# Kernel optimization log

Hardware: AMD Instinct MI355X
Metric: run time of the kernel (lower is better)

The kernel has to match this reference:

```python
import jax, jax.numpy as jnp
import numpy as np

B, T, C, H = 4, 2048, 1024, 16
HS = C // H  # head dim = 64
EPS = 1e-5


def _layernorm(h, w, b):
    m = jnp.mean(h, axis=-1, keepdims=True)
    v = jnp.mean(jnp.square(h - m), axis=-1, keepdims=True)
    return (h - m) * jax.lax.rsqrt(v + EPS) * w + b


def _quantize_int8(t):
    # per-tensor absmax int8 quantization, matching the torch code
    absmax = jnp.max(jnp.abs(t))
    scale = jnp.where(absmax > 0, absmax / 127.0, jnp.float32(1.0))
    q = jnp.clip(jnp.round(t / scale), -127, 127).astype(jnp.int8)
    return q, scale


def setup_inputs() -> dict:
    key = jax.random.key(0)
    ks = jax.random.split(key, 8)
    w = lambda k, shape: (jax.random.normal(k, shape, jnp.float32) * 0.02)
    return {
        "x": jax.random.normal(ks[0], (B, T, C), jnp.float32),
        "ln1_w": jnp.ones((C,), jnp.float32),
        "ln1_b": jnp.zeros((C,), jnp.float32),
        "W_qkv": w(ks[1], (C, 3 * C)),
        "b_qkv": jnp.zeros((3 * C,), jnp.float32),
        "W_o": w(ks[2], (C, C)),
        "b_o": jnp.zeros((C,), jnp.float32),
        "ln2_w": jnp.ones((C,), jnp.float32),
        "ln2_b": jnp.zeros((C,), jnp.float32),
        "W_fc": w(ks[3], (C, 4 * C)),
        "b_fc": jnp.zeros((4 * C,), jnp.float32),
        "W_pr": w(ks[4], (4 * C, C)),
        "b_pr": jnp.zeros((C,), jnp.float32),
    }


def reference(x, ln1_w, ln1_b, W_qkv, b_qkv, W_o, b_o, ln2_w, ln2_b, W_fc, b_fc, W_pr, b_pr):
    # ---- attention (prefill, cache-owner, kv_cache_quant=True, use_cache=True) ----
    h = _layernorm(x, ln1_w, ln1_b)
    qkv = h @ W_qkv + b_qkv                       # (B,T,3C)
    q, k, v = jnp.split(qkv, 3, axis=-1)
    q = q.reshape(B, T, H, HS).transpose(0, 2, 1, 3)  # (B,H,T,hs)
    k = k.reshape(B, T, H, HS).transpose(0, 2, 1, 3)
    v = v.reshape(B, T, H, HS).transpose(0, 2, 1, 3)

    # quantized `present` cache (returned, not used for attention in prefill path)
    k_quant, k_scale = _quantize_int8(k)
    v_quant, v_scale = _quantize_int8(v)

    # causal SDPA (dropout=0)
    att = jnp.einsum("bhqd,bhkd->bhqk", q, k) * (1.0 / np.sqrt(HS))
    causal = jnp.tril(jnp.ones((T, T), bool))
    att = jnp.where(causal[None, None], att, jnp.float32(-jnp.inf))
    att = jax.nn.softmax(att, axis=-1)
    y = jnp.einsum("bhqk,bhkd->bhqd", att, v)
    y = y.transpose(0, 2, 1, 3).reshape(B, T, C)
    y = y @ W_o + b_o
    x = x + y

    # ---- MLP ----
    h2 = _layernorm(x, ln2_w, ln2_b)
    h2 = jax.nn.gelu(h2 @ W_fc + b_fc, approximate=False)
    x = x + (h2 @ W_pr + b_pr)

    return x, k_quant, k_scale, v_quant, v_scale
```

## Files before the change

### kernel.cpp

```cpp
#include <hip/hip_runtime.h>
#include <cmath>

typedef __bf16 bf16;
typedef float f32x4 __attribute__((ext_vector_type(4)));
typedef __bf16 bf16x4 __attribute__((ext_vector_type(4)));
typedef __bf16 bf16x8 __attribute__((ext_vector_type(8)));

#define DEVI __device__ __forceinline__

constexpr int Bn = 4, Tn = 2048, Cn = 1024, Hn = 16, HSn = 64;
constexpr int C3n = 3 * Cn;
constexpr int BTn = Bn * Tn;

constexpr size_t OFF_WT_QKV = 0;
constexpr size_t OFF_WT_O   = 6291456;
constexpr size_t OFF_WT_FC  = 8388608;
constexpr size_t OFF_WT_PR  = 16777216;
constexpr size_t OFF_H      = 25165824;
constexpr size_t OFF_Y      = 41943040;
constexpr size_t OFF_X1     = 58720256;
constexpr size_t OFF_AMAX   = 92274688;
constexpr size_t OFF_QKV    = 92274944;
constexpr size_t OFF_G      = OFF_QKV;

constexpr size_t OUT_X  = 0;
constexpr size_t OUT_KQ = 8388608;
constexpr size_t OUT_KS = 16777216;
constexpr size_t OUT_VQ = 16777217;
constexpr size_t OUT_VS = 25165825;

DEVI void g2l16(const void* g, void* l) {
  __builtin_amdgcn_global_load_lds(
      (__attribute__((address_space(1))) void*)g,
      (__attribute__((address_space(3))) void*)l, 16, 0, 0);
}

DEVI float gelu_f(float x) {
  const float ax = fabsf(x) * 0.7071067811865476f;
  const float t = 1.0f / (1.0f + 0.3275911f * ax);
  const float p = t * (0.254829592f + t * (-0.284496736f +
                  t * (1.421413741f + t * (-1.453152027f + t * 1.061405429f))));
  float er = 1.0f - p * __expf(-ax * ax);
  er = (x < 0.0f) ? -er : er;
  return 0.5f * x * (1.0f + er);
}

struct TrJob { const float* W; bf16* Wt; int K, N, bx; };

__global__ __launch_bounds__(256) void k_prep(const float* W0, bf16* T0,
                                              const float* W1, bf16* T1,
                                              const float* W2, bf16* T2,
                                              const float* W3, bf16* T3,
                                              unsigned int* amax) {
  __shared__ float tile[32][33];
  const int id = blockIdx.x;
  if (id == 0 && threadIdx.x == 0 && threadIdx.y == 0) { amax[0] = 0u; amax[1] = 0u; }

  const float* W; bf16* Wt; int K, N, lid;
  if (id < 3072)      { W = W0; Wt = T0; K = 1024; N = 3072; lid = id; }
  else if (id < 4096) { W = W1; Wt = T1; K = 1024; N = 1024; lid = id - 3072; }
  else if (id < 8192) { W = W2; Wt = T2; K = 1024; N = 4096; lid = id - 4096; }
  else                { W = W3; Wt = T3; K = 4096; N = 1024; lid = id - 8192; }
  const int gx = N >> 5;
  const int n0 = (lid % gx) * 32, k0 = (lid / gx) * 32;
  const int tx = threadIdx.x, ty = threadIdx.y;
#pragma unroll
  for (int i = 0; i < 4; ++i) {
    int k = k0 + ty + i * 8;
    tile[ty + i * 8][tx] = W[(size_t)k * N + (n0 + tx)];
  }
  __syncthreads();
#pragma unroll
  for (int i = 0; i < 4; ++i) {
    int n = n0 + ty + i * 8;
    Wt[(size_t)n * K + (k0 + tx)] = (bf16)tile[tx][ty + i * 8];
  }
}

__global__ __launch_bounds__(256) void k_ln(const float* __restrict__ x,
                                            const float* __restrict__ g,
                                            const float* __restrict__ b,
                                            bf16* __restrict__ out) {
  __shared__ float red[8];
  const int row = blockIdx.x, tid = threadIdx.x;
  const int lane = tid & 63, wv = tid >> 6;
  f32x4 v = ((const f32x4*)(x + (size_t)row * Cn))[tid];

  float s = v[0] + v[1] + v[2] + v[3];
  s += __shfl_down(s, 32); s += __shfl_down(s, 16); s += __shfl_down(s, 8);
  s += __shfl_down(s, 4);  s += __shfl_down(s, 2);  s += __shfl_down(s, 1);
  if (!lane) red[wv] = s;
  __syncthreads();
  const float mean = (red[0] + red[1] + red[2] + red[3]) * (1.0f / 1024.0f);
  __syncthreads();

  f32x4 d = v - mean;
  float s2 = d[0]*d[0] + d[1]*d[1] + d[2]*d[2] + d[3]*d[3];
  s2 += __shfl_down(s2, 32); s2 += __shfl_down(s2, 16); s2 += __shfl_down(s2, 8);
  s2 += __shfl_down(s2, 4);  s2 += __shfl_down(s2, 2);  s2 += __shfl_down(s2, 1);
  if (!lane) red[wv] = s2;
  __syncthreads();
  const float var = (red[0] + red[1] + red[2] + red[3]) * (1.0f / 1024.0f);
  const float inv = rsqrtf(var + 1e-5f);

  f32x4 gw = ((const f32x4*)g)[tid];
  f32x4 bb = ((const f32x4*)b)[tid];
  bf16x4 o;
#pragma unroll
  for (int j = 0; j < 4; ++j) o[j] = (bf16)(d[j] * inv * gw[j] + bb[j]);
  *(bf16x4*)(out + (size_t)row * Cn + tid * 4) = o;
}

#define VMCNT(N) asm volatile("s_waitcnt vmcnt(" #N ")" ::: "memory")
#define LGKM0()  asm volatile("s_waitcnt lgkmcnt(0)" ::: "memory")
#define BARW()   asm volatile("s_barrier" ::: "memory")

DEVI void stage_half(const bf16* __restrict__ G, int ldk, int row0, int k0,
                     bf16* dst, int w, int lane) {
  const int srow = lane >> 3;
  const int sch = ((lane & 7) ^ srow) * 8;
  const bf16* src = G + (size_t)(row0 + srow) * ldk + k0 + sch;
#pragma unroll
  for (int i = 0; i < 2; ++i) {
    const int g = 2 * w + i;
    g2l16(src + (size_t)(8 * g) * ldk, dst + g * 512);
  }
}

DEVI void read_b(const bf16* BsB, int wn, int l15, int quad, bf16x8 (&bv)[2][2]) {
#pragma unroll
  for (int nt = 0; nt < 2; ++nt)
#pragma unroll
    for (int kk = 0; kk < 2; ++kk) {
      const int row = wn * 32 + nt * 16 + l15;
      const int c = ((kk * 4 + quad) ^ (l15 & 7)) * 8;
      bv[nt][kk] = *(const bf16x8*)(BsB + row * 64 + c);
    }
}

template <int Q>
DEVI void read_aq(const bf16* AsB, int wm, int l15, int quad, bf16x8 (&af)[2]) {
#pragma unroll
  for (int kk = 0; kk < 2; ++kk) {
    const int row = wm * 64 + Q * 16 + l15;
    const int c = ((kk * 4 + quad) ^ (l15 & 7)) * 8;
    af[kk] = *(const bf16x8*)(AsB + row * 64 + c);
  }
}

template <int Q>
DEVI void mfma_q(const bf16x8 (&af)[2], const bf16x8 (&bv)[2][2],
                 f32x4 (&acc)[4][2]) {
#pragma unroll
  for (int nt = 0; nt < 2; ++nt)
#pragma unroll
    for (int kk = 0; kk < 2; ++kk)
      acc[Q][nt] = __builtin_amdgcn_mfma_f32_16x16x32_bf16(
          af[kk], bv[nt][kk], acc[Q][nt], 0, 0, 0);
}

template <int BUF>
DEVI void tile_iter(int kt, int kIters, const bf16* __restrict__ A,
                    const bf16* __restrict__ Bt, int K, int m0, int n0,
                    bf16* As0, bf16* As1, bf16* Bs0, bf16* Bs1,
                    f32x4 (&acc)[4][2], int w, int lane) {
  const int l15 = lane & 15, quad = lane >> 4;
  const int wm = w >> 2, wn = w & 3;
  const bf16* AsB = BUF ? As1 : As0;
  const bf16* BsB = BUF ? Bs1 : Bs0;
  bf16* AsW = BUF ? As1 : As0;
  bf16* BsW = BUF ? Bs1 : Bs0;

  bf16x8 bv[2][2];
  bf16x8 af0[2], af1[2], af2[2], af3[2];

  read_b(BsB, wn, l15, quad, bv);
  read_aq<0>(AsB, wm, l15, quad, af0);
  read_aq<1>(AsB, wm, l15, quad, af1);
  read_aq<2>(AsB, wm, l15, quad, af2);
  read_aq<3>(AsB, wm, l15, quad, af3);
  mfma_q<0>(af0, bv, acc);
  mfma_q<1>(af1, bv, acc);

  LGKM0();
  BARW();

  if (kt + 2 < kIters) {
    stage_half(A,  K, m0, (kt + 2) * 64, AsW, w, lane);
    stage_half(Bt, K, n0, (kt + 2) * 64, BsW, w, lane);
  }
  mfma_q<2>(af2, bv, acc);
  mfma_q<3>(af3, bv, acc);
  if (kt + 2 < kIters) {
    VMCNT(4);
    BARW();
  } else if (kt + 1 < kIters) {
    VMCNT(0);
    BARW();
  }
}

template <bool RES, bool GELU, bool AMAX, bool F32OUT>
__global__ __launch_bounds__(512, 4) void k_gemmT(const bf16* __restrict__ A,
                                                  const bf16* __restrict__ Bt,
                                                  const float* __restrict__ bias,
                                                  const float* __restrict__ res,
                                                  void* __restrict__ Cout,
                                                  unsigned int* __restrict__ amax,
                                                  int M, int N, int K) {
  __shared__ bf16 As0[128 * 64], As1[128 * 64];
  __shared__ bf16 Bs0[128 * 64], Bs1[128 * 64];
  __shared__ float redA[8];
  const int tid = threadIdx.x;
  const int lane = tid & 63, w = tid >> 6;
  const int wm = w >> 2, wn = w & 3;
  const int l15 = lane & 15, quad = lane >> 4;
  const int m0 = blockIdx.x * 128, n0 = blockIdx.y * 128;
  const int kIters = K >> 6;
  (void)M;

  stage_half(A,  K, m0, 0,  As0, w, lane);
  stage_half(Bt, K, n0, 0,  Bs0, w, lane);
  stage_half(A,  K, m0, 64, As1, w, lane);
  stage_half(Bt, K, n0, 64, Bs1, w, lane);
  VMCNT(4);
  BARW();

  f32x4 acc[4][2] = {};

  const int nPairs = kIters >> 1;
  for (int p = 0; p < nPairs; ++p) {
    tile_iter<0>(2 * p,     kIters, A, Bt, K, m0, n0, As0, As1, Bs0, Bs1, acc, w, lane);
    tile_iter<1>(2 * p + 1, kIters, A, Bt, K, m0, n0, As0, As1, Bs0, Bs1, acc, w, lane);
  }

  const int colB = n0 + wn * 32 + l15;
  const int rowB = m0 + wm * 64 + (quad << 2);
  float lm = 0.0f;
#pragma unroll
  for (int mt = 0; mt < 4; ++mt) {
#pragma unroll
    for (int nt = 0; nt < 2; ++nt) {
      const int col = colB + nt * 16;
      const float bval = bias[col];
#pragma unroll
      for (int r = 0; r < 4; ++r) {
        const int row = rowB + mt * 16 + r;
        float val = acc[mt][nt][r] + bval;
        if (GELU) val = gelu_f(val);
        if (RES)  val += res[(size_t)row * N + col];
        if (AMAX) lm = fmaxf(lm, fabsf(val));
        if (F32OUT) ((float*)Cout)[(size_t)row * N + col] = val;
        else        ((bf16*)Cout)[(size_t)row * N + col] = (bf16)val;
      }
    }
  }

  if (AMAX) {
    const int cls = n0 >> 10;
    if (cls > 0) {
      lm = fmaxf(lm, __shfl_xor(lm, 1));
      lm = fmaxf(lm, __shfl_xor(lm, 2));
      lm = fmaxf(lm, __shfl_xor(lm, 4));
      lm = fmaxf(lm, __shfl_xor(lm, 8));
      lm = fmaxf(lm, __shfl_xor(lm, 16));
      lm = fmaxf(lm, __shfl_xor(lm, 32));
      if (!lane) redA[w] = lm;
      __syncthreads();
      if (tid == 0) {
        float m8 = redA[0];
#pragma unroll
        for (int i = 1; i < 8; ++i) m8 = fmaxf(m8, redA[i]);
        atomicMax(amax + (cls - 1), __float_as_uint(m8));
      }
    }
  }
}

__global__ __launch_bounds__(256) void k_quant(const bf16* __restrict__ qkv,
                                               const unsigned int* __restrict__ amax,
                                               float* __restrict__ out) {
  const float ka = __uint_as_float(amax[0]);
  const float va = __uint_as_float(amax[1]);
  const float ks = ka > 0.0f ? ka / 127.0f : 1.0f;
  const float vs = va > 0.0f ? va / 127.0f : 1.0f;
  if (blockIdx.x == 0 && threadIdx.x == 0) { out[OUT_KS] = ks; out[OUT_VS] = vs; }
  const float kinv = 1.0f / ks, vinv = 1.0f / vs;
  const size_t nchunks = 1048576;
  const size_t stride = (size_t)gridDim.x * blockDim.x;
  for (size_t ci = (size_t)blockIdx.x * blockDim.x + threadIdx.x; ci < nchunks; ci += stride) {
    const int d0 = (int)(ci & 7) * 8;
    const int t  = (int)(ci >> 3) & 2047;
    const int h  = (int)(ci >> 14) & 15;
    const int b  = (int)(ci >> 18);
    const size_t src = ((size_t)(b * Tn + t)) * C3n + h * HSn + d0;
    bf16x8 k8 = *(const bf16x8*)(qkv + src + Cn);
    bf16x8 v8 = *(const bf16x8*)(qkv + src + 2 * Cn);
    float kq[8], vq[8];
#pragma unroll
    for (int j = 0; j < 8; ++j) {
      kq[j] = fminf(fmaxf(rintf((float)k8[j] * kinv), -127.0f), 127.0f);
      vq[j] = fminf(fmaxf(rintf((float)v8[j] * vinv), -127.0f), 127.0f);
    }
    const size_t oi = ci * 8;
    f32x4 a0 = {kq[0], kq[1], kq[2], kq[3]};
    f32x4 a1 = {kq[4], kq[5], kq[6], kq[7]};
    *(f32x4*)(out + OUT_KQ + oi)     = a0;
    *(f32x4*)(out + OUT_KQ + oi + 4) = a1;
    float* vdst = out + OUT_VQ + oi;
#pragma unroll
    for (int j = 0; j < 8; ++j) vdst[j] = vq[j];
  }
}

__global__ __launch_bounds__(256, 3) void k_attn(const bf16* __restrict__ qkv,
                                                 bf16* __restrict__ y) {
  __shared__ bf16 Ks[2][64 * 64];
  __shared__ bf16 Vt[2][64 * 64];
  __shared__ bf16 Pt[4][2][16 * 64];

  const int tid = threadIdx.x;
  const int lane = tid & 63;
  const int w = tid >> 6;
  const int quad = lane >> 4;
  const int l15 = lane & 15;

  const int bh = blockIdx.x;
  const int qt = 15 - (int)blockIdx.y;
  const int b = bh >> 4, h = bh & 15;
  const int q0 = qt * 128;
  const int ktMax = 2 * qt + 1;

  const bf16* qkv_b = qkv + (size_t)b * Tn * C3n + h * HSn;
  const bf16* kbase = qkv_b + Cn;
  const bf16* vbase = qkv_b + 2 * Cn;

  const int srow = lane >> 3;
  const int schunk = ((lane & 7) ^ srow) * 8;

  const bf16* q0p = qkv_b + (size_t)(q0 + 16 * w + l15) * C3n;
  const bf16* q1p = q0p + (size_t)64 * C3n;
  bf16x8 qf[2][2];
  qf[0][0] = *(const bf16x8*)(q0p + quad * 8);
  qf[0][1] = *(const bf16x8*)(q0p + 32 + quad * 8);
  qf[1][0] = *(const bf16x8*)(q1p + quad * 8);
  qf[1][1] = *(const bf16x8*)(q1p + 32 + quad * 8);

  g2l16(kbase + (size_t)(8 * w + srow) * C3n + schunk, (bf16*)Ks[0] + w * 512);
  g2l16(kbase + (size_t)(8 * (w + 4) + srow) * C3n + schunk, (bf16*)Ks[0] + (w + 4) * 512);
  bf16x8 v0 = *(const bf16x8*)(vbase + (size_t)lane * C3n + w * 8);
  bf16x8 v1 = *(const bf16x8*)(vbase + (size_t)lane * C3n + (w + 4) * 8);
  __builtin_amdgcn_s_waitcnt(0);
#pragma unroll
  for (int j = 0; j < 8; ++j) {
    Vt[0][(w * 8 + j) * 64 + ((srow ^ j) << 3) + (lane & 7)] = v0[j];
    Vt[0][((w + 4) * 8 + j) * 64 + ((srow ^ j) << 3) + (lane & 7)] = v1[j];
  }
  __syncthreads();

  f32x4 Od[2][4] = {};
  float m_i[2] = {-INFINITY, -INFINITY};
  float l_i[2] = {0.0f, 0.0f};

  for (int kt = 0; kt <= ktMax; ++kt) {
    const int bsel = kt & 1;

    bf16x8 nv0, nv1;
    if (kt < ktMax) {
      const int kv1 = (kt + 1) * 64;
      g2l16(kbase + (size_t)(kv1 + 8 * w + srow) * C3n + schunk,
            (bf16*)Ks[bsel ^ 1] + w * 512);
      g2l16(kbase + (size_t)(kv1 + 8 * (w + 4) + srow) * C3n + schunk,
            (bf16*)Ks[bsel ^ 1] + (w + 4) * 512);
      nv0 = *(const bf16x8*)(vbase + (size_t)(kv1 + lane) * C3n + w * 8);
      nv1 = *(const bf16x8*)(vbase + (size_t)(kv1 + lane) * C3n + (w + 4) * 8);
    }

    const bf16* KsB = Ks[bsel];
    f32x4 S0[4] = {}, S1[4] = {};
#pragma unroll
    for (int ks = 0; ks < 2; ++ks)
#pragma unroll
      for (int nt = 0; nt < 4; ++nt) {
        const int rn = nt * 16 + l15;
        const int c = ((ks * 4 + quad) ^ (l15 & 7)) * 8;
        bf16x8 kf = *(const bf16x8*)(KsB + rn * 64 + c);
        S0[nt] = __builtin_amdgcn_mfma_f32_16x16x32_bf16(kf, qf[0][ks], S0[nt], 0, 0, 0);
        S1[nt] = __builtin_amdgcn_mfma_f32_16x16x32_bf16(kf, qf[1][ks], S1[nt], 0, 0, 0);
      }

    const int qloc = 16 * w + l15;
    const int th[2] = { kt < 2 * qt ? 64 : (kt == 2 * qt ? qloc : -1),
                        kt < ktMax ? 64 : qloc };
    f32x4* Sg[2] = {S0, S1};
#pragma unroll
    for (int g = 0; g < 2; ++g) {
      float s[4][4];
      float mx = -INFINITY;
#pragma unroll
      for (int nt = 0; nt < 4; ++nt)
#pragma unroll
        for (int r = 0; r < 4; ++r) {
          float v = Sg[g][nt][r] * 0.125f;
          if (nt * 16 + quad * 4 + r > th[g]) v = -INFINITY;
          s[nt][r] = v;
          mx = fmaxf(mx, v);
        }
      mx = fmaxf(mx, __shfl_xor(mx, 16));
      mx = fmaxf(mx, __shfl_xor(mx, 32));
      const float mn = fmaxf(m_i[g], mx);
      const float al = __expf(m_i[g] - mn);
      m_i[g] = mn;
      float rsum = 0.0f;
      bf16x4 pk[4];
#pragma unroll
      for (int nt = 0; nt < 4; ++nt)
#pragma unroll
        for (int r = 0; r < 4; ++r) {
          const float p = __expf(s[nt][r] - mn);
          rsum += p;
          pk[nt][r] = (bf16)p;
        }
      rsum += __shfl_xor(rsum, 16);
      rsum += __shfl_xor(rsum, 32);
      l_i[g] = l_i[g] * al + rsum;
#pragma unroll
      for (int dt = 0; dt < 4; ++dt) Od[g][dt] *= al;
#pragma unroll
      for (int nt = 0; nt < 4; ++nt) {
        const int phys = (nt * 2 + (quad >> 1)) ^ (l15 & 7);
        *(bf16x4*)(&Pt[w][g][0] + l15 * 64 + phys * 8 + (quad & 1) * 4) = pk[nt];
      }
    }

    const bf16* VtB = Vt[bsel];
#pragma unroll
    for (int ks2 = 0; ks2 < 2; ++ks2) {
      const int pc = ((ks2 * 4 + quad) ^ (l15 & 7)) * 8;
      bf16x8 pf0 = *(const bf16x8*)(&Pt[w][0][0] + l15 * 64 + pc);
      bf16x8 pf1 = *(const bf16x8*)(&Pt[w][1][0] + l15 * 64 + pc);
#pragma unroll
      for (int dt = 0; dt < 4; ++dt) {
        const int d = dt * 16 + l15;
        bf16x8 vf = *(const bf16x8*)(VtB + d * 64 + pc);
        Od[0][dt] = __builtin_amdgcn_mfma_f32_16x16x32_bf16(vf, pf0, Od[0][dt], 0, 0, 0);
        Od[1][dt] = __builtin_amdgcn_mfma_f32_16x16x32_bf16(vf, pf1, Od[1][dt], 0, 0, 0);
      }
    }

    if (kt < ktMax) {
      __builtin_amdgcn_s_waitcnt(0);
#pragma unroll
      for (int j = 0; j < 8; ++j) {
        Vt[bsel ^ 1][(w * 8 + j) * 64 + ((srow ^ j) << 3) + (lane & 7)] = nv0[j];
        Vt[bsel ^ 1][((w + 4) * 8 + j) * 64 + ((srow ^ j) << 3) + (lane & 7)] = nv1[j];
      }
      __syncthreads();
    }
  }

#pragma unroll
  for (int g = 0; g < 2; ++g) {
    const float invl = 1.0f / l_i[g];
    const size_t yb = ((size_t)b * Tn + q0 + g * 64 + 16 * w + l15) * Cn + h * HSn;
#pragma unroll
    for (int dt = 0; dt < 4; ++dt) {
      bf16x4 o;
#pragma unroll
      for (int r = 0; r < 4; ++r) o[r] = (bf16)(Od[g][dt][r] * invl);
      *(bf16x4*)(y + yb + dt * 16 + quad * 4) = o;
    }
  }
}

extern "C" void kernel_launch(void* const* d_in, const int* in_sizes, int n_in,
                              void* d_out, int out_size, void* d_ws, size_t ws_size,
                              hipStream_t stream) {
  const float* x     = (const float*)d_in[0];
  const float* ln1w  = (const float*)d_in[1];
  const float* ln1b  = (const float*)d_in[2];
  const float* Wqkv  = (const float*)d_in[3];
  const float* bqkv  = (const float*)d_in[4];
  const float* Wo    = (const float*)d_in[5];
  const float* bo    = (const float*)d_in[6];
  const float* ln2w  = (const float*)d_in[7];
  const float* ln2b  = (const float*)d_in[8];
  const float* Wfc   = (const float*)d_in[9];
  const float* bfc   = (const float*)d_in[10];
  const float* Wpr   = (const float*)d_in[11];
  const float* bpr   = (const float*)d_in[12];

  char* ws = (char*)d_ws;
  bf16*  Wt_qkv = (bf16*)(ws + OFF_WT_QKV);
  bf16*  Wt_o   = (bf16*)(ws + OFF_WT_O);
  bf16*  Wt_fc  = (bf16*)(ws + OFF_WT_FC);
  bf16*  Wt_pr  = (bf16*)(ws + OFF_WT_PR);
  bf16*  h      = (bf16*)(ws + OFF_H);
  bf16*  ybf    = (bf16*)(ws + OFF_Y);
  float* x1     = (float*)(ws + OFF_X1);
  unsigned int* amax = (unsigned int*)(ws + OFF_AMAX);
  bf16*  qkvbf  = (bf16*)(ws + OFF_QKV);
  bf16*  g      = (bf16*)(ws + OFF_G);
  float* out    = (float*)d_out;

  k_prep<<<dim3(12288), dim3(32, 8), 0, stream>>>(Wqkv, Wt_qkv, Wo, Wt_o,
                                                  Wfc, Wt_fc, Wpr, Wt_pr, amax);

  k_ln<<<BTn, 256, 0, stream>>>(x, ln1w, ln1b, h);
  k_gemmT<false, false, true, false><<<dim3(64, 24), 512, 0, stream>>>(
      h, Wt_qkv, bqkv, nullptr, qkvbf, amax, 8192, 3072, 1024);
  k_quant<<<2048, 256, 0, stream>>>(qkvbf, amax, out);
  k_attn<<<dim3(64, 16), 256, 0, stream>>>(qkvbf, ybf);
  k_gemmT<true, false, false, true><<<dim3(64, 8), 512, 0, stream>>>(
      ybf, Wt_o, bo, x, x1, nullptr, 8192, 1024, 1024);
  k_ln<<<BTn, 256, 0, stream>>>(x1, ln2w, ln2b, h);
  k_gemmT<false, true, false, false><<<dim3(64, 32), 512, 0, stream>>>(
      h, Wt_fc, bfc, nullptr, g, nullptr, 8192, 4096, 1024);
  k_gemmT<true, false, false, true><<<dim3(64, 8), 512, 0, stream>>>(
      g, Wt_pr, bpr, x1, out, nullptr, 8192, 1024, 4096);
}
```

Baseline: 523.0 us.

## Widen GEMM tile to 128x256 with register double-buffered fragment prefetch

The GEMM block tile grows from 128x128 to 128x256, so each wave computes a 64x64 sub-tile with 16 accumulators instead of 8. This raises MFMA work per LDS fragment load and cuts the grid size for every projection GEMM. The main loop also moves to a software pipeline: the fragments for the next k-step are read from LDS into a second register set while the MFMAs for the current step run. The cost is more registers and LDS (launch bounds drop to 2 blocks per SM) and fewer blocks per GEMM, which can hurt occupancy and load balance, especially for the N=1024 GEMMs that now launch only 256 blocks.

```diff
diff --git a/kernel.cpp b/kernel.cpp
--- a/kernel.cpp
+++ b/kernel.cpp
@@ -45,8 +45,6 @@
   return 0.5f * x * (1.0f + er);
 }
 
-struct TrJob { const float* W; bf16* Wt; int K, N, bx; };
-
 __global__ __launch_bounds__(256) void k_prep(const float* W0, bf16* T0,
                                               const float* W1, bf16* T1,
                                               const float* W2, bf16* T2,
@@ -115,93 +113,66 @@
 #define LGKM0()  asm volatile("s_waitcnt lgkmcnt(0)" ::: "memory")
 #define BARW()   asm volatile("s_barrier" ::: "memory")
 
-DEVI void stage_half(const bf16* __restrict__ G, int ldk, int row0, int k0,
-                     bf16* dst, int w, int lane) {
+template <int NG>
+DEVI void stageN(const bf16* __restrict__ G, int ldk, int row0, int k0,
+                 bf16* dst, int w, int lane) {
   const int srow = lane >> 3;
   const int sch = ((lane & 7) ^ srow) * 8;
   const bf16* src = G + (size_t)(row0 + srow) * ldk + k0 + sch;
 #pragma unroll
-  for (int i = 0; i < 2; ++i) {
-    const int g = 2 * w + i;
+  for (int i = 0; i < NG; ++i) {
+    const int g = NG * w + i;
     g2l16(src + (size_t)(8 * g) * ldk, dst + g * 512);
   }
 }
 
-DEVI void read_b(const bf16* BsB, int wn, int l15, int quad, bf16x8 (&bv)[2][2]) {
-#pragma unroll
-  for (int nt = 0; nt < 2; ++nt)
+DEVI void read_frags(const bf16* AsB, const bf16* BsB, int wm, int wn,
+                     int l15, int quad, bf16x8 (&af)[4][2], bf16x8 (&bv)[4][2]) {
+#pragma unroll
+  for (int q = 0; q < 4; ++q)
 #pragma unroll
     for (int kk = 0; kk < 2; ++kk) {
-      const int row = wn * 32 + nt * 16 + l15;
       const int c = ((kk * 4 + quad) ^ (l15 & 7)) * 8;
-      bv[nt][kk] = *(const bf16x8*)(BsB + row * 64 + c);
-    }
-}
-
-template <int Q>
-DEVI void read_aq(const bf16* AsB, int wm, int l15, int quad, bf16x8 (&af)[2]) {
-#pragma unroll
-  for (int kk = 0; kk < 2; ++kk) {
-    const int row = wm * 64 + Q * 16 + l15;
-    const int c = ((kk * 4 + quad) ^ (l15 & 7)) * 8;
-    af[kk] = *(const bf16x8*)(AsB + row * 64 + c);
-  }
-}
-
-template <int Q>
-DEVI void mfma_q(const bf16x8 (&af)[2], const bf16x8 (&bv)[2][2],
-                 f32x4 (&acc)[4][2]) {
-#pragma unroll
-  for (int nt = 0; nt < 2; ++nt)
-#pragma unroll
-    for (int kk = 0; kk < 2; ++kk)
-      acc[Q][nt] = __builtin_amdgcn_mfma_f32_16x16x32_bf16(
-          af[kk], bv[nt][kk], acc[Q][nt], 0, 0, 0);
-}
-
-template <int BUF>
-DEVI void tile_iter(int kt, int kIters, const bf16* __restrict__ A,
+      af[q][kk] = *(const bf16x8*)(AsB + (wm * 64 + q * 16 + l15) * 64 + c);
+      bv[q][kk] = *(const bf16x8*)(BsB + (wn * 64 + q * 16 + l15) * 64 + c);
+    }
+}
+
+DEVI void mfma_all(const bf16x8 (&af)[4][2], const bf16x8 (&bv)[4][2],
+                   f32x4 (&acc)[4][4]) {
+#pragma unroll
+  for (int mt = 0; mt < 4; ++mt)
+#pragma unroll
+    for (int nt = 0; nt < 4; ++nt)
+#pragma unroll
+      for (int kk = 0; kk < 2; ++kk)
+        acc[mt][nt] = __builtin_amdgcn_mfma_f32_16x16x32_bf16(
+            af[mt][kk], bv[nt][kk], acc[mt][nt], 0, 0, 0);
+}
+
+DEVI void gemm_iter(int kt, int kIters, const bf16* __restrict__ A,
                     const bf16* __restrict__ Bt, int K, int m0, int n0,
-                    bf16* As0, bf16* As1, bf16* Bs0, bf16* Bs1,
-                    f32x4 (&acc)[4][2], int w, int lane) {
-  const int l15 = lane & 15, quad = lane >> 4;
-  const int wm = w >> 2, wn = w & 3;
-  const bf16* AsB = BUF ? As1 : As0;
-  const bf16* BsB = BUF ? Bs1 : Bs0;
-  bf16* AsW = BUF ? As1 : As0;
-  bf16* BsW = BUF ? Bs1 : Bs0;
-
-  bf16x8 bv[2][2];
-  bf16x8 af0[2], af1[2], af2[2], af3[2];
-
-  read_b(BsB, wn, l15, quad, bv);
-  read_aq<0>(AsB, wm, l15, quad, af0);
-  read_aq<1>(AsB, wm, l15, quad, af1);
-  read_aq<2>(AsB, wm, l15, quad, af2);
-  read_aq<3>(AsB, wm, l15, quad, af3);
-  mfma_q<0>(af0, bv, acc);
-  mfma_q<1>(af1, bv, acc);
-
+                    bf16* AsW, bf16* BsW, const bf16* AsR, const bf16* BsR,
+                    bf16x8 (&afC)[4][2], bf16x8 (&bvC)[4][2],
+                    bf16x8 (&afN)[4][2], bf16x8 (&bvN)[4][2],
+                    f32x4 (&acc)[4][4], int w, int lane, int wm, int wn) {
+  if (kt + 2 < kIters) {
+    stageN<2>(A,  K, m0, (kt + 2) * 64, AsW, w, lane);
+    stageN<4>(Bt, K, n0, (kt + 2) * 64, BsW, w, lane);
+    VMCNT(6);
+  } else {
+    VMCNT(0);
+  }
+  BARW();
+  if (kt + 1 < kIters)
+    read_frags(AsR, BsR, wm, wn, lane & 15, lane >> 4, afN, bvN);
+  mfma_all(afC, bvC, acc);
   LGKM0();
   BARW();
-
-  if (kt + 2 < kIters) {
-    stage_half(A,  K, m0, (kt + 2) * 64, AsW, w, lane);
-    stage_half(Bt, K, n0, (kt + 2) * 64, BsW, w, lane);
-  }
-  mfma_q<2>(af2, bv, acc);
-  mfma_q<3>(af3, bv, acc);
-  if (kt + 2 < kIters) {
-    VMCNT(4);
-    BARW();
-  } else if (kt + 1 < kIters) {
-    VMCNT(0);
-    BARW();
-  }
 }
 
 template <bool RES, bool GELU, bool AMAX, bool F32OUT>
-__global__ __launch_bounds__(512, 4) void k_gemmT(const bf16* __restrict__ A,
+__global__ __launch_bounds__(512, 2) void k_gemmT(const bf16* __restrict__ A,
                                                   const bf16* __restrict__ Bt,
                                                   const float* __restrict__ bias,
                                                   const float* __restrict__ res,
@@ -209,38 +180,45 @@
                                                   unsigned int* __restrict__ amax,
                                                   int M, int N, int K) {
   __shared__ bf16 As0[128 * 64], As1[128 * 64];
-  __shared__ bf16 Bs0[128 * 64], Bs1[128 * 64];
+  __shared__ bf16 Bs0[256 * 64], Bs1[256 * 64];
   __shared__ float redA[8];
   const int tid = threadIdx.x;
   const int lane = tid & 63, w = tid >> 6;
   const int wm = w >> 2, wn = w & 3;
   const int l15 = lane & 15, quad = lane >> 4;
-  const int m0 = blockIdx.x * 128, n0 = blockIdx.y * 128;
+  const int m0 = blockIdx.x * 128, n0 = blockIdx.y * 256;
   const int kIters = K >> 6;
   (void)M;
 
-  stage_half(A,  K, m0, 0,  As0, w, lane);
-  stage_half(Bt, K, n0, 0,  Bs0, w, lane);
-  stage_half(A,  K, m0, 64, As1, w, lane);
-  stage_half(Bt, K, n0, 64, Bs1, w, lane);
-  VMCNT(4);
+  stageN<2>(A,  K, m0, 0,  As0, w, lane);
+  stageN<4>(Bt, K, n0, 0,  Bs0, w, lane);
+  stageN<2>(A,  K, m0, 64, As1, w, lane);
+  stageN<4>(Bt, K, n0, 64, Bs1, w, lane);
+  VMCNT(6);
   BARW();
 
-  f32x4 acc[4][2] = {};
+  bf16x8 afE[4][2], bvE[4][2], afO[4][2], bvO[4][2];
+  read_frags(As0, Bs0, wm, wn, l15, quad, afE, bvE);
+  LGKM0();
+  BARW();
+
+  f32x4 acc[4][4] = {};
 
   const int nPairs = kIters >> 1;
   for (int p = 0; p < nPairs; ++p) {
-    tile_iter<0>(2 * p,     kIters, A, Bt, K, m0, n0, As0, As1, Bs0, Bs1, acc, w, lane);
-    tile_iter<1>(2 * p + 1, kIters, A, Bt, K, m0, n0, As0, As1, Bs0, Bs1, acc, w, lane);
-  }
-
-  const int colB = n0 + wn * 32 + l15;
+    gemm_iter(2 * p,     kIters, A, Bt, K, m0, n0, As0, Bs0, As1, Bs1,
+              afE, bvE, afO, bvO, acc, w, lane, wm, wn);
+    gemm_iter(2 * p + 1, kIters, A, Bt, K, m0, n0, As1, Bs1, As0, Bs0,
+              afO, bvO, afE, bvE, acc, w, lane, wm, wn);
+  }
+
+  const int colB = n0 + wn * 64 + l15;
   const int rowB = m0 + wm * 64 + (quad << 2);
   float lm = 0.0f;
 #pragma unroll
   for (int mt = 0; mt < 4; ++mt) {
 #pragma unroll
-    for (int nt = 0; nt < 2; ++nt) {
+    for (int nt = 0; nt < 4; ++nt) {
       const int col = colB + nt * 16;
       const float bval = bias[col];
 #pragma unroll
@@ -507,15 +485,15 @@
                                                   Wfc, Wt_fc, Wpr, Wt_pr, amax);
 
   k_ln<<<BTn, 256, 0, stream>>>(x, ln1w, ln1b, h);
-  k_gemmT<false, false, true, false><<<dim3(64, 24), 512, 0, stream>>>(
+  k_gemmT<false, false, true, false><<<dim3(64, 12), 512, 0, stream>>>(
       h, Wt_qkv, bqkv, nullptr, qkvbf, amax, 8192, 3072, 1024);
   k_quant<<<2048, 256, 0, stream>>>(qkvbf, amax, out);
   k_attn<<<dim3(64, 16), 256, 0, stream>>>(qkvbf, ybf);
-  k_gemmT<true, false, false, true><<<dim3(64, 8), 512, 0, stream>>>(
+  k_gemmT<true, false, false, true><<<dim3(64, 4), 512, 0, stream>>>(
       ybf, Wt_o, bo, x, x1, nullptr, 8192, 1024, 1024);
   k_ln<<<BTn, 256, 0, stream>>>(x1, ln2w, ln2b, h);
-  k_gemmT<false, true, false, false><<<dim3(64, 32), 512, 0, stream>>>(
+  k_gemmT<false, true, false, false><<<dim3(64, 16), 512, 0, stream>>>(
       h, Wt_fc, bfc, nullptr, g, nullptr, 8192, 4096, 1024);
-  k_gemmT<true, false, false, true><<<dim3(64, 8), 512, 0, stream>>>(
+  k_gemmT<true, false, false, true><<<dim3(64, 4), 512, 0, stream>>>(
       g, Wt_pr, bpr, x1, out, nullptr, 8192, 1024, 4096);
 }
```

New measurement: 527.8 us. No clear change (+0.9%).
